# Performance work log

Measured on AMD Instinct MI355X. Metric: run time of the kernel, lower is better.

The kernel has to match this reference:

```python
import jax, jax.numpy as jnp
import numpy as np

ALPHA = 0.95
BETA = 0.9

def setup_inputs() -> dict:
    key = jax.random.key(0)
    k1, k2 = jax.random.split(key)
    B, T, I, O = 64, 1000, 512, 256
    inputs = jax.random.normal(k1, (B, T, I), dtype=jnp.float32)
    W = jax.random.normal(k2, (O, I), dtype=jnp.float32) * (1.0 / np.sqrt(I))
    return {"inputs": inputs, "W": W, "nb_steps": T}

def reference(inputs, W, nb_steps):
    B = inputs.shape[0]
    O = W.shape[0]
    # linear projection: h[b,t,o]
    h = jnp.einsum('bti,oi->bto', inputs, W)
    h_t = jnp.swapaxes(h, 0, 1)  # (T, B, O) for scan over time

    def step(carry, ht):
        flt, out = carry
        new_flt = ALPHA * flt + ht
        new_out = BETA * out + flt  # uses OLD flt, matching the torch loop
        return (new_flt, new_out), new_out

    init = (jnp.zeros((B, O), jnp.float32), jnp.zeros((B, O), jnp.float32))
    _, out_rec = jax.lax.scan(step, init, h_t)
    return jnp.swapaxes(out_rec, 0, 1)  # (B, T, O)
```

## Files before the change

kernel.cpp:

```cpp
#include <hip/hip_runtime.h>
#include <stdint.h>


#define ALPHA 0.95f
#define BETA  0.9f

constexpr int Bdim = 64, T = 1000, Idim = 512, Odim = 256;
constexpr int M = Bdim * T;
constexpr int C = 40, L = 25;
constexpr int BO = Bdim * Odim;

typedef short bf16x8 __attribute__((ext_vector_type(8)));
typedef float f32x4  __attribute__((ext_vector_type(4)));

__device__ inline uint32_t pk_bf16(float a, float b) {
  union { float f; uint32_t u; } x, y; x.f = a; y.f = b;
  uint32_t lo = (x.u + 0x7FFFu + ((x.u >> 16) & 1u)) >> 16;
  uint32_t hi = (y.u + 0x7FFFu + ((y.u >> 16) & 1u)) & 0xFFFF0000u;
  return lo | hi;
}
__device__ inline uint16_t f2bf(float a) {
  union { float f; uint32_t u; } x; x.f = a;
  return (uint16_t)((x.u + 0x7FFFu + ((x.u >> 16) & 1u)) >> 16);
}
__device__ inline float bf2f(uint16_t h) {
  union { uint32_t u; float f; } x; x.u = ((uint32_t)h) << 16;
  return x.f;
}

__global__ __launch_bounds__(256, 2) void gemm_h(const float* __restrict__ A,
                                                 const float* __restrict__ W,
                                                 uint16_t* __restrict__ H) {
  __shared__ uint16_t Wl[64 * 512];

  const int tid  = threadIdx.x;
  const int lane = tid & 63;
  const int wave = tid >> 6;
  const int l15  = lane & 15;
  const int quad = lane >> 4;
  const int cn   = blockIdx.x * 64;
  const int rm   = blockIdx.y * 256;

  {
    const int r  = tid >> 2;
    const int cb = (tid & 3) * 16;
    const float* wr = W + (size_t)(cn + r) * Idim;
#pragma unroll
    for (int i = 0; i < 16; ++i) {
      int c = cb + i;
      float4 lo = *(const float4*)(wr + c * 8);
      float4 hi = *(const float4*)(wr + c * 8 + 4);
      *(uint4*)&Wl[r * 512 + ((c ^ (r & 7)) * 8)] =
          make_uint4(pk_bf16(lo.x, lo.y), pk_bf16(lo.z, lo.w),
                     pk_bf16(hi.x, hi.y), pk_bf16(hi.z, hi.w));
    }
  }
  __syncthreads();

  const float* ar[4];
#pragma unroll
  for (int mt = 0; mt < 4; ++mt)
    ar[mt] = A + (size_t)(rm + wave * 64 + mt * 16 + l15) * Idim + quad * 8;

  f32x4 acc[4][4] = {};

  float4 cur[4][2];
#pragma unroll
  for (int mt = 0; mt < 4; ++mt) {
    cur[mt][0] = *(const float4*)(ar[mt]);
    cur[mt][1] = *(const float4*)(ar[mt] + 4);
  }

#pragma unroll
  for (int ks = 0; ks < 16; ++ks) {
    float4 nxt[4][2];
    if (ks < 15) {
#pragma unroll
      for (int mt = 0; mt < 4; ++mt) {
        nxt[mt][0] = *(const float4*)(ar[mt] + (ks + 1) * 32);
        nxt[mt][1] = *(const float4*)(ar[mt] + (ks + 1) * 32 + 4);
      }
    }
    bf16x8 bfr[4];
#pragma unroll
    for (int nt = 0; nt < 4; ++nt)
      bfr[nt] = *(const bf16x8*)&Wl[(nt * 16 + l15) * 512 + (((ks * 4 + quad) ^ (l15 & 7)) * 8)];
    bf16x8 af[4];
#pragma unroll
    for (int mt = 0; mt < 4; ++mt) {
      union { uint4 u; bf16x8 v; } t;
      t.u = make_uint4(pk_bf16(cur[mt][0].x, cur[mt][0].y), pk_bf16(cur[mt][0].z, cur[mt][0].w),
                       pk_bf16(cur[mt][1].x, cur[mt][1].y), pk_bf16(cur[mt][1].z, cur[mt][1].w));
      af[mt] = t.v;
    }
#pragma unroll
    for (int mt = 0; mt < 4; ++mt)
#pragma unroll
      for (int nt = 0; nt < 4; ++nt)
        acc[mt][nt] = __builtin_amdgcn_mfma_f32_16x16x32_bf16(af[mt], bfr[nt], acc[mt][nt], 0, 0, 0);
    if (ks < 15) {
#pragma unroll
      for (int mt = 0; mt < 4; ++mt) { cur[mt][0] = nxt[mt][0]; cur[mt][1] = nxt[mt][1]; }
    }
  }

#pragma unroll
  for (int mt = 0; mt < 4; ++mt)
#pragma unroll
    for (int nt = 0; nt < 4; ++nt)
#pragma unroll
      for (int r = 0; r < 4; ++r) {
        int gm = rm + wave * 64 + mt * 16 + quad * 4 + r;
        int gn = cn + nt * 16 + l15;
        H[(size_t)gm * Odim + gn] = f2bf(acc[mt][nt][r]);
      }
}

__global__ __launch_bounds__(256) void scan_local(const uint16_t* __restrict__ H,
                                                  float2* __restrict__ St) {
  const int pair = blockIdx.x * 4 + (threadIdx.x >> 6);
  const int b = pair / C, c = pair % C;
  const int lane = threadIdx.x & 63;
  const ushort4* hp = (const ushort4*)(H + (size_t)(b * T + c * L) * Odim) + lane;
  float f[4] = {}, u[4] = {};
#pragma unroll
  for (int j = 0; j < L; ++j) {
    ushort4 hv = hp[j * 64];
    float h0 = bf2f(hv.x), h1 = bf2f(hv.y), h2 = bf2f(hv.z), h3 = bf2f(hv.w);
    float n0 = BETA * u[0] + f[0]; f[0] = ALPHA * f[0] + h0; u[0] = n0;
    float n1 = BETA * u[1] + f[1]; f[1] = ALPHA * f[1] + h1; u[1] = n1;
    float n2 = BETA * u[2] + f[2]; f[2] = ALPHA * f[2] + h2; u[2] = n2;
    float n3 = BETA * u[3] + f[3]; f[3] = ALPHA * f[3] + h3; u[3] = n3;
  }
  float2* sp = &St[(size_t)c * BO + b * Odim + lane * 4];
#pragma unroll
  for (int i = 0; i < 4; ++i) sp[i] = make_float2(f[i], u[i]);
}

constexpr double dpow(double x, int n) { double r = 1.0; for (int i = 0; i < n; ++i) r *= x; return r; }

__global__ __launch_bounds__(256) void scan_combine(const float2* __restrict__ St,
                                                    float2* __restrict__ Init) {
  constexpr float AL = (float)dpow(0.95, L);
  constexpr float BL = (float)dpow(0.90, L);
  constexpr float WL = (float)((dpow(0.95, L) - dpow(0.90, L)) / (0.95 - 0.90));
  const int i = blockIdx.x * 256 + threadIdx.x;
  float f = 0.f, u = 0.f;
#pragma unroll
  for (int c = 0; c < C; ++c) {
    Init[(size_t)c * BO + i] = make_float2(f, u);
    float2 s = St[(size_t)c * BO + i];
    float nf = AL * f + s.x;
    float nu = BL * u + WL * f + s.y;
    f = nf; u = nu;
  }
}

__global__ __launch_bounds__(256) void scan_final(const uint16_t* __restrict__ H,
                                                  const float2* __restrict__ Init,
                                                  float* __restrict__ Out) {
  const int pair = blockIdx.x * 4 + (threadIdx.x >> 6);
  const int b = pair / C, c = pair % C;
  const int lane = threadIdx.x & 63;
  const size_t base = (size_t)(b * T + c * L) * Odim;
  const ushort4* hp = (const ushort4*)(H + base) + lane;
  float4* op = (float4*)(Out + base) + lane;
  const float2* sp = &Init[(size_t)c * BO + b * Odim + lane * 4];
  float f[4], u[4];
#pragma unroll
  for (int i = 0; i < 4; ++i) { float2 s = sp[i]; f[i] = s.x; u[i] = s.y; }
#pragma unroll
  for (int j = 0; j < L; ++j) {
    ushort4 hv = hp[j * 64];
    float h0 = bf2f(hv.x), h1 = bf2f(hv.y), h2 = bf2f(hv.z), h3 = bf2f(hv.w);
    float4 o4;
    o4.x = BETA * u[0] + f[0]; f[0] = ALPHA * f[0] + h0; u[0] = o4.x;
    o4.y = BETA * u[1] + f[1]; f[1] = ALPHA * f[1] + h1; u[1] = o4.y;
    o4.z = BETA * u[2] + f[2]; f[2] = ALPHA * f[2] + h2; u[2] = o4.z;
    o4.w = BETA * u[3] + f[3]; f[3] = ALPHA * f[3] + h3; u[3] = o4.w;
    op[j * 64] = o4;
  }
}

extern "C" void kernel_launch(void* const* d_in, const int* in_sizes, int n_in,
                              void* d_out, int out_size, void* d_ws, size_t ws_size,
                              hipStream_t stream) {
  const float* A = (const float*)d_in[0];
  const float* W = (const float*)d_in[1];
  float* Out = (float*)d_out;

  uint16_t* H = (uint16_t*)d_ws;
  const size_t hbytes = (size_t)M * Odim * sizeof(uint16_t);
  float2* St   = (float2*)((char*)d_ws + hbytes);
  float2* Init = St + (size_t)C * BO;

  gemm_h<<<dim3(Odim / 64, M / 256), 256, 0, stream>>>(A, W, H);
  scan_local<<<Bdim * C / 4, 256, 0, stream>>>(H, St);
  scan_combine<<<BO / 256, 256, 0, stream>>>(St, Init);
  scan_final<<<Bdim * C / 4, 256, 0, stream>>>(H, Init, Out);
}
```

Measured before the change: 274.7 us.

## Restructure GEMM with LDS async loads and fuse three scan kernels into one

Converts W to bf16 once in a separate kernel, then rewrites the GEMM so each block covers 64 rows by all 256 outputs. A and W tiles are staged through LDS with global_load_lds in 32-wide k-steps, and A is read from HBM only once instead of four times. The three scan kernels (local, combine, final) become one kernel per (batch, 64-output group), with chunk states combined in shared memory instead of round-tripping through global memory. Risks: the GEMM loop is no longer software-pipelined, with two barriers per k-step, and the fused scan runs only 256 blocks, so its parallelism is limited.

```diff
diff --git a/kernel.cpp b/kernel.cpp
--- a/kernel.cpp
+++ b/kernel.cpp
@@ -1,4 +1,5 @@
 #include <hip/hip_runtime.h>
+#include <hip/hip_bf16.h>
 #include <stdint.h>
 
 
@@ -8,7 +9,6 @@
 constexpr int Bdim = 64, T = 1000, Idim = 512, Odim = 256;
 constexpr int M = Bdim * T;
 constexpr int C = 40, L = 25;
-constexpr int BO = Bdim * Odim;
 
 typedef short bf16x8 __attribute__((ext_vector_type(8)));
 typedef float f32x4  __attribute__((ext_vector_type(4)));
@@ -28,80 +28,92 @@
   return x.f;
 }
 
-__global__ __launch_bounds__(256, 2) void gemm_h(const float* __restrict__ A,
-                                                 const float* __restrict__ W,
-                                                 uint16_t* __restrict__ H) {
-  __shared__ uint16_t Wl[64 * 512];
+#define GLD16(g, l) __builtin_amdgcn_global_load_lds(                         \
+    (const __attribute__((address_space(1))) uint32_t*)(g),                   \
+    (__attribute__((address_space(3))) uint32_t*)(l), 16, 0, 0)
+
+__device__ inline bf16x8 cvt8(float4 x0, float4 x1) {
+  union { __hip_bfloat162 h[4]; bf16x8 v; } r;
+  r.h[0] = __float22bfloat162_rn(make_float2(x0.x, x0.y));
+  r.h[1] = __float22bfloat162_rn(make_float2(x0.z, x0.w));
+  r.h[2] = __float22bfloat162_rn(make_float2(x1.x, x1.y));
+  r.h[3] = __float22bfloat162_rn(make_float2(x1.z, x1.w));
+  return r.v;
+}
+
+__global__ __launch_bounds__(256) void wconv(const float* __restrict__ W,
+                                             uint16_t* __restrict__ Wbf) {
+  int i = (blockIdx.x * 256 + threadIdx.x) * 8;
+  float4 a = *(const float4*)(W + i);
+  float4 b = *(const float4*)(W + i + 4);
+  *(uint4*)(Wbf + i) = make_uint4(pk_bf16(a.x, a.y), pk_bf16(a.z, a.w),
+                                  pk_bf16(b.x, b.y), pk_bf16(b.z, b.w));
+}
+
+__global__ __launch_bounds__(256) void gemm_h(const float* __restrict__ A,
+                                              const uint16_t* __restrict__ Wbf,
+                                              uint16_t* __restrict__ H) {
+  __shared__ float    As[64 * 32];
+  __shared__ uint16_t Bs[256 * 32];
 
   const int tid  = threadIdx.x;
   const int lane = tid & 63;
-  const int wave = tid >> 6;
+  const int w    = tid >> 6;
   const int l15  = lane & 15;
   const int quad = lane >> 4;
-  const int cn   = blockIdx.x * 64;
-  const int rm   = blockIdx.y * 256;
-
-  {
-    const int r  = tid >> 2;
-    const int cb = (tid & 3) * 16;
-    const float* wr = W + (size_t)(cn + r) * Idim;
-#pragma unroll
-    for (int i = 0; i < 16; ++i) {
-      int c = cb + i;
-      float4 lo = *(const float4*)(wr + c * 8);
-      float4 hi = *(const float4*)(wr + c * 8 + 4);
-      *(uint4*)&Wl[r * 512 + ((c ^ (r & 7)) * 8)] =
-          make_uint4(pk_bf16(lo.x, lo.y), pk_bf16(lo.z, lo.w),
-                     pk_bf16(hi.x, hi.y), pk_bf16(hi.z, hi.w));
-    }
-  }
-  __syncthreads();
-
-  const float* ar[4];
-#pragma unroll
-  for (int mt = 0; mt < 4; ++mt)
-    ar[mt] = A + (size_t)(rm + wave * 64 + mt * 16 + l15) * Idim + quad * 8;
+  const int rm   = blockIdx.x * 64;
+
+  const int ar = w * 8 + (lane >> 3);
+  const int akc = (lane & 7) ^ ((lane >> 3) & 7);
+  const int br = w * 16 + (lane >> 2);
+  const int bkc = (lane & 3) ^ ((lane >> 2) & 3);
+
+  const float*    ag0 = A   + (size_t)(rm + ar) * Idim + akc * 4;
+  const float*    ag1 = A   + (size_t)(rm + 32 + ar) * Idim + akc * 4;
+  const uint16_t* bg[4];
+#pragma unroll
+  for (int p = 0; p < 4; ++p) bg[p] = Wbf + (size_t)(p * 64 + br) * Idim + bkc * 8;
+
+  char* al0 = (char*)As + w * 1024;
+  char* al1 = (char*)As + 4096 + w * 1024;
+  char* bl[4];
+#pragma unroll
+  for (int p = 0; p < 4; ++p) bl[p] = (char*)Bs + p * 4096 + w * 1024;
+
+  int aoff0[4], aoff1[4], boff[4];
+#pragma unroll
+  for (int t = 0; t < 4; ++t) {
+    int m = t * 16 + l15;
+    aoff0[t] = m * 32 + (((2 * quad)     ^ (m & 7)) * 4);
+    aoff1[t] = m * 32 + (((2 * quad + 1) ^ (m & 7)) * 4);
+    int n = w * 64 + t * 16 + l15;
+    boff[t] = n * 32 + ((quad ^ (n & 3)) * 8);
+  }
 
   f32x4 acc[4][4] = {};
 
-  float4 cur[4][2];
-#pragma unroll
-  for (int mt = 0; mt < 4; ++mt) {
-    cur[mt][0] = *(const float4*)(ar[mt]);
-    cur[mt][1] = *(const float4*)(ar[mt] + 4);
-  }
-
-#pragma unroll
-  for (int ks = 0; ks < 16; ++ks) {
-    float4 nxt[4][2];
-    if (ks < 15) {
-#pragma unroll
-      for (int mt = 0; mt < 4; ++mt) {
-        nxt[mt][0] = *(const float4*)(ar[mt] + (ks + 1) * 32);
-        nxt[mt][1] = *(const float4*)(ar[mt] + (ks + 1) * 32 + 4);
-      }
-    }
-    bf16x8 bfr[4];
-#pragma unroll
-    for (int nt = 0; nt < 4; ++nt)
-      bfr[nt] = *(const bf16x8*)&Wl[(nt * 16 + l15) * 512 + (((ks * 4 + quad) ^ (l15 & 7)) * 8)];
-    bf16x8 af[4];
-#pragma unroll
-    for (int mt = 0; mt < 4; ++mt) {
-      union { uint4 u; bf16x8 v; } t;
-      t.u = make_uint4(pk_bf16(cur[mt][0].x, cur[mt][0].y), pk_bf16(cur[mt][0].z, cur[mt][0].w),
-                       pk_bf16(cur[mt][1].x, cur[mt][1].y), pk_bf16(cur[mt][1].z, cur[mt][1].w));
-      af[mt] = t.v;
-    }
+  for (int k0 = 0; k0 < Idim; k0 += 32) {
+    __syncthreads();
+    GLD16(ag0 + k0, al0);
+    GLD16(ag1 + k0, al1);
+#pragma unroll
+    for (int p = 0; p < 4; ++p) GLD16(bg[p] + k0, bl[p]);
+    __syncthreads();
+
+    bf16x8 af[4], bfr[4];
+#pragma unroll
+    for (int t = 0; t < 4; ++t) {
+      float4 x0 = *(const float4*)&As[aoff0[t]];
+      float4 x1 = *(const float4*)&As[aoff1[t]];
+      af[t] = cvt8(x0, x1);
+    }
+#pragma unroll
+    for (int t = 0; t < 4; ++t) bfr[t] = *(const bf16x8*)&Bs[boff[t]];
 #pragma unroll
     for (int mt = 0; mt < 4; ++mt)
 #pragma unroll
       for (int nt = 0; nt < 4; ++nt)
         acc[mt][nt] = __builtin_amdgcn_mfma_f32_16x16x32_bf16(af[mt], bfr[nt], acc[mt][nt], 0, 0, 0);
-    if (ks < 15) {
-#pragma unroll
-      for (int mt = 0; mt < 4; ++mt) { cur[mt][0] = nxt[mt][0]; cur[mt][1] = nxt[mt][1]; }
-    }
   }
 
 #pragma unroll
@@ -110,75 +122,75 @@
     for (int nt = 0; nt < 4; ++nt)
 #pragma unroll
       for (int r = 0; r < 4; ++r) {
-        int gm = rm + wave * 64 + mt * 16 + quad * 4 + r;
-        int gn = cn + nt * 16 + l15;
+        int gm = rm + mt * 16 + quad * 4 + r;
+        int gn = w * 64 + nt * 16 + l15;
         H[(size_t)gm * Odim + gn] = f2bf(acc[mt][nt][r]);
       }
 }
 
-__global__ __launch_bounds__(256) void scan_local(const uint16_t* __restrict__ H,
-                                                  float2* __restrict__ St) {
-  const int pair = blockIdx.x * 4 + (threadIdx.x >> 6);
-  const int b = pair / C, c = pair % C;
-  const int lane = threadIdx.x & 63;
-  const ushort4* hp = (const ushort4*)(H + (size_t)(b * T + c * L) * Odim) + lane;
-  float f[4] = {}, u[4] = {};
-#pragma unroll
-  for (int j = 0; j < L; ++j) {
-    ushort4 hv = hp[j * 64];
-    float h0 = bf2f(hv.x), h1 = bf2f(hv.y), h2 = bf2f(hv.z), h3 = bf2f(hv.w);
-    float n0 = BETA * u[0] + f[0]; f[0] = ALPHA * f[0] + h0; u[0] = n0;
-    float n1 = BETA * u[1] + f[1]; f[1] = ALPHA * f[1] + h1; u[1] = n1;
-    float n2 = BETA * u[2] + f[2]; f[2] = ALPHA * f[2] + h2; u[2] = n2;
-    float n3 = BETA * u[3] + f[3]; f[3] = ALPHA * f[3] + h3; u[3] = n3;
-  }
-  float2* sp = &St[(size_t)c * BO + b * Odim + lane * 4];
-#pragma unroll
-  for (int i = 0; i < 4; ++i) sp[i] = make_float2(f[i], u[i]);
-}
-
 constexpr double dpow(double x, int n) { double r = 1.0; for (int i = 0; i < n; ++i) r *= x; return r; }
 
-__global__ __launch_bounds__(256) void scan_combine(const float2* __restrict__ St,
-                                                    float2* __restrict__ Init) {
+__global__ __launch_bounds__(640) void scan_all(const uint16_t* __restrict__ H,
+                                                float* __restrict__ Out) {
   constexpr float AL = (float)dpow(0.95, L);
   constexpr float BL = (float)dpow(0.90, L);
   constexpr float WL = (float)((dpow(0.95, L) - dpow(0.90, L)) / (0.95 - 0.90));
-  const int i = blockIdx.x * 256 + threadIdx.x;
-  float f = 0.f, u = 0.f;
-#pragma unroll
-  for (int c = 0; c < C; ++c) {
-    Init[(size_t)c * BO + i] = make_float2(f, u);
-    float2 s = St[(size_t)c * BO + i];
-    float nf = AL * f + s.x;
-    float nu = BL * u + WL * f + s.y;
-    f = nf; u = nu;
-  }
-}
-
-__global__ __launch_bounds__(256) void scan_final(const uint16_t* __restrict__ H,
-                                                  const float2* __restrict__ Init,
-                                                  float* __restrict__ Out) {
-  const int pair = blockIdx.x * 4 + (threadIdx.x >> 6);
-  const int b = pair / C, c = pair % C;
-  const int lane = threadIdx.x & 63;
-  const size_t base = (size_t)(b * T + c * L) * Odim;
-  const ushort4* hp = (const ushort4*)(H + base) + lane;
-  float4* op = (float4*)(Out + base) + lane;
-  const float2* sp = &Init[(size_t)c * BO + b * Odim + lane * 4];
-  float f[4], u[4];
-#pragma unroll
-  for (int i = 0; i < 4; ++i) { float2 s = sp[i]; f[i] = s.x; u[i] = s.y; }
-#pragma unroll
-  for (int j = 0; j < L; ++j) {
-    ushort4 hv = hp[j * 64];
-    float h0 = bf2f(hv.x), h1 = bf2f(hv.y), h2 = bf2f(hv.z), h3 = bf2f(hv.w);
-    float4 o4;
-    o4.x = BETA * u[0] + f[0]; f[0] = ALPHA * f[0] + h0; u[0] = o4.x;
-    o4.y = BETA * u[1] + f[1]; f[1] = ALPHA * f[1] + h1; u[1] = o4.y;
-    o4.z = BETA * u[2] + f[2]; f[2] = ALPHA * f[2] + h2; u[2] = o4.z;
-    o4.w = BETA * u[3] + f[3]; f[3] = ALPHA * f[3] + h3; u[3] = o4.w;
-    op[j * 64] = o4;
+  __shared__ float2 St[C][64];
+
+  const int b  = blockIdx.x >> 2;
+  const int og = blockIdx.x & 3;
+  const int tid = threadIdx.x;
+  const int c  = tid >> 4;
+  const int ol = tid & 15;
+
+  const size_t base = ((size_t)b * T + c * L) * Odim + og * 64 + ol * 4;
+  const ushort4* hp = (const ushort4*)(H + base);
+
+  {
+    float f[4] = {}, u[4] = {};
+#pragma unroll
+    for (int j = 0; j < L; ++j) {
+      ushort4 hv = hp[j * 64];
+      float h0 = bf2f(hv.x), h1 = bf2f(hv.y), h2 = bf2f(hv.z), h3 = bf2f(hv.w);
+      float n0 = BETA * u[0] + f[0]; f[0] = ALPHA * f[0] + h0; u[0] = n0;
+      float n1 = BETA * u[1] + f[1]; f[1] = ALPHA * f[1] + h1; u[1] = n1;
+      float n2 = BETA * u[2] + f[2]; f[2] = ALPHA * f[2] + h2; u[2] = n2;
+      float n3 = BETA * u[3] + f[3]; f[3] = ALPHA * f[3] + h3; u[3] = n3;
+    }
+#pragma unroll
+    for (int i = 0; i < 4; ++i) St[c][ol * 4 + i] = make_float2(f[i], u[i]);
+  }
+  __syncthreads();
+
+  if (tid < 64) {
+    float f = 0.f, u = 0.f;
+#pragma unroll
+    for (int cc = 0; cc < C; ++cc) {
+      float2 s = St[cc][tid];
+      St[cc][tid] = make_float2(f, u);
+      float nu = BL * u + WL * f + s.y;
+      f = AL * f + s.x;
+      u = nu;
+    }
+  }
+  __syncthreads();
+
+  {
+    float f[4], u[4];
+#pragma unroll
+    for (int i = 0; i < 4; ++i) { float2 s = St[c][ol * 4 + i]; f[i] = s.x; u[i] = s.y; }
+    float4* op = (float4*)(Out + base);
+#pragma unroll
+    for (int j = 0; j < L; ++j) {
+      ushort4 hv = hp[j * 64];
+      float h0 = bf2f(hv.x), h1 = bf2f(hv.y), h2 = bf2f(hv.z), h3 = bf2f(hv.w);
+      float4 o4;
+      o4.x = BETA * u[0] + f[0]; f[0] = ALPHA * f[0] + h0; u[0] = o4.x;
+      o4.y = BETA * u[1] + f[1]; f[1] = ALPHA * f[1] + h1; u[1] = o4.y;
+      o4.z = BETA * u[2] + f[2]; f[2] = ALPHA * f[2] + h2; u[2] = o4.z;
+      o4.w = BETA * u[3] + f[3]; f[3] = ALPHA * f[3] + h3; u[3] = o4.w;
+      op[j * 64] = o4;
+    }
   }
 }
 
@@ -189,13 +201,10 @@
   const float* W = (const float*)d_in[1];
   float* Out = (float*)d_out;
 
-  uint16_t* H = (uint16_t*)d_ws;
-  const size_t hbytes = (size_t)M * Odim * sizeof(uint16_t);
-  float2* St   = (float2*)((char*)d_ws + hbytes);
-  float2* Init = St + (size_t)C * BO;
-
-  gemm_h<<<dim3(Odim / 64, M / 256), 256, 0, stream>>>(A, W, H);
-  scan_local<<<Bdim * C / 4, 256, 0, stream>>>(H, St);
-  scan_combine<<<BO / 256, 256, 0, stream>>>(St, Init);
-  scan_final<<<Bdim * C / 4, 256, 0, stream>>>(H, Init, Out);
-}
+  uint16_t* H   = (uint16_t*)d_ws;
+  uint16_t* Wbf = H + (size_t)M * Odim;
+
+  wconv<<<Odim * Idim / (256 * 8), 256, 0, stream>>>(W, Wbf);
+  gemm_h<<<M / 64, 256, 0, stream>>>(A, Wbf, H);
+  scan_all<<<Bdim * 4, 640, 0, stream>>>(H, Out);
+}
```

After: 247.2 us. 1.11x faster.
